# Kernel tuning notes

Measured on AMD Instinct MI355X. Metric: run time of the kernel, lower is better.

Reference implementation:

```python
import jax, jax.numpy as jnp
import numpy as np

B, L, D, H = 8, 512, 1024, 16
HD = D // H
DIST_VOCAB = 64
NEG = -1e9


def setup_inputs() -> dict:
    key = jax.random.key(0)
    ks = jax.random.split(key, 16)
    inp = {}
    inp['q'] = jax.random.normal(ks[0], (B, L, D), jnp.float32)
    inp['k'] = jax.random.normal(ks[1], (B, L, D), jnp.float32)
    inp['v'] = jax.random.normal(ks[2], (B, L, D), jnp.float32)
    s = 1.0 / np.sqrt(D)
    inp['Wq'] = jax.random.normal(ks[3], (D, D), jnp.float32) * s
    inp['bq'] = jnp.zeros((D,), jnp.float32)
    inp['Wk'] = jax.random.normal(ks[4], (D, D), jnp.float32) * s
    inp['bk'] = jnp.zeros((D,), jnp.float32)
    inp['Wv'] = jax.random.normal(ks[5], (D, D), jnp.float32) * s
    inp['bv'] = jnp.zeros((D,), jnp.float32)
    inp['Wo'] = jax.random.normal(ks[6], (D, D), jnp.float32) * s
    inp['bo'] = jnp.zeros((D,), jnp.float32)
    inp['dist_emb'] = jax.random.normal(ks[7], (DIST_VOCAB, H), jnp.float32) * (1.0 / np.sqrt(H))
    # sinusoidal positional table (1, L, D), rank-3 as asserted in AttentionBase
    pos = np.arange(L)[:, None]
    dim = np.arange(D)[None, :]
    ang = pos / np.power(10000.0, (2 * (dim // 2)) / D)
    pe = np.where(dim % 2 == 0, np.sin(ang), np.cos(ang)).astype(np.float32)
    inp['sin_enc'] = jnp.asarray(pe)[None]
    inp['length'] = jax.random.randint(ks[8], (B,), L // 2, L + 1, jnp.int32)
    inp['dist'] = jax.random.randint(ks[9], (B, L, L), 0, DIST_VOCAB, jnp.int32)
    return inp


def _rope(x, sin_pos, cos_pos):
    # x: (B, L, D). rotate-half interleaved: [-x1, x0, -x3, x2, ...]
    x_shift = jnp.stack([-x[..., 1::2], x[..., 0::2]], axis=-1).reshape(x.shape)
    return x * cos_pos + x_shift * sin_pos


def reference(q, k, v, Wq, bq, Wk, bk, Wv, bv, Wo, bo, dist_emb, sin_enc, length, dist):
    # linear projections (torch Linear: x @ W.T + b)
    qp = q @ Wq.T + bq
    kp = k @ Wk.T + bk
    vp = v @ Wv.T + bv
    # rope (pe='rope', cls_len=0, step=0)
    sin_pos = jnp.repeat(sin_enc[:, :L, 0::2], 2, axis=-1)
    cos_pos = jnp.repeat(sin_enc[:, :L, 1::2], 2, axis=-1)
    qp = _rope(qp, sin_pos, cos_pos)
    kp = _rope(kp, sin_pos, cos_pos)
    # split heads -> (B, H, L, HD)
    qh = qp.reshape(B, L, H, HD).transpose(0, 2, 1, 3)
    kh = kp.reshape(B, L, H, HD).transpose(0, 2, 1, 3)
    vh = vp.reshape(B, L, H, HD).transpose(0, 2, 1, 3)
    # scale (scale_length=0 -> 1/sqrt(d_head))
    qh = qh * (1.0 / np.sqrt(HD))
    scores = jnp.einsum('bhqd,bhkd->bhqk', qh, kh)
    # relative 'dist' bias: (B,L,L,H) -> (B,H,L,L)
    scores = scores + dist_emb[dist].transpose(0, 3, 1, 2)
    # padding mask: key positions >= valid length (future=False)
    key_mask = jnp.arange(L)[None, :] >= length[:, None]  # (B, L)
    scores = jnp.where(key_mask[:, None, None, :], NEG, scores)
    attn = jax.nn.softmax(scores, axis=-1)  # dropout p=0.0 => identity
    out = jnp.einsum('bhqk,bhkd->bhqd', attn, vh)
    out = out.transpose(0, 2, 1, 3).reshape(B, L, D)
    return out @ Wo.T + bo
```

## Files before the change

### kernel.cpp

```cpp
#include <hip/hip_runtime.h>
#include <stdint.h>

typedef unsigned short u16;
typedef __bf16 bf16x8 __attribute__((ext_vector_type(8)));
typedef float f32x4 __attribute__((ext_vector_type(4)));

#define MFMA16(a, b, c) __builtin_amdgcn_mfma_f32_16x16x32_bf16(a, b, c, 0, 0, 0)

__device__ __forceinline__ float b2f(u16 u) { return __uint_as_float(((uint32_t)u) << 16); }
__device__ __forceinline__ u16 f2b(float f) {
    uint32_t x = __float_as_uint(f);
    return (u16)((x + 0x7fffu + ((x >> 16) & 1u)) >> 16);
}
__device__ __forceinline__ void load16(const void* g, void* l) {
    __builtin_amdgcn_global_load_lds(
        (const __attribute__((address_space(1))) uint32_t*)(uintptr_t)g,
        (__attribute__((address_space(3))) uint32_t*)(uint32_t)(uintptr_t)l,
        16, 0, 0);
}
__device__ __forceinline__ bf16x8 ld8f(const float* f) {
    float4 a = *(const float4*)f;
    float4 b = *(const float4*)(f + 4);
    bf16x8 o;
    o[0] = (__bf16)a.x; o[1] = (__bf16)a.y; o[2] = (__bf16)a.z; o[3] = (__bf16)a.w;
    o[4] = (__bf16)b.x; o[5] = (__bf16)b.y; o[6] = (__bf16)b.z; o[7] = (__bf16)b.w;
    return o;
}

__global__ __launch_bounds__(256) void convert_k(
    const float* __restrict__ q, const float* __restrict__ k, const float* __restrict__ v,
    const float* __restrict__ Wq, const float* __restrict__ Wk,
    const float* __restrict__ Wv, const float* __restrict__ Wo,
    u16* __restrict__ qb, u16* __restrict__ kb, u16* __restrict__ vb,
    u16* __restrict__ wqb, u16* __restrict__ wkb, u16* __restrict__ wvb,
    u16* __restrict__ wob)
{
    const float* src; u16* dst; int n8;
    switch (blockIdx.y) {
        case 0: src = q;  dst = qb;  n8 = 524288; break;
        case 1: src = k;  dst = kb;  n8 = 524288; break;
        case 2: src = v;  dst = vb;  n8 = 524288; break;
        case 3: src = Wq; dst = wqb; n8 = 131072; break;
        case 4: src = Wk; dst = wkb; n8 = 131072; break;
        case 5: src = Wv; dst = wvb; n8 = 131072; break;
        default: src = Wo; dst = wob; n8 = 131072; break;
    }
    int i = blockIdx.x * 256 + threadIdx.x;
    if (i >= n8) return;
    bf16x8 o = ld8f(src + (size_t)i * 8);
    *(bf16x8*)(dst + (size_t)i * 8) = o;
}

__global__ __launch_bounds__(256, 6) void gemm_proj_b(
    const u16* __restrict__ qb, const u16* __restrict__ kb, const u16* __restrict__ vb,
    const u16* __restrict__ wqb, const u16* __restrict__ wkb, const u16* __restrict__ wvb,
    const float* __restrict__ bq, const float* __restrict__ bk, const float* __restrict__ bv,
    const float* __restrict__ sin_enc,
    u16* __restrict__ qh, u16* __restrict__ kh, u16* __restrict__ vt)
{
    __shared__ __align__(16) u16 lA[2][64 * 32];
    __shared__ __align__(16) u16 lB[2][128 * 32];
    const int t = threadIdx.x, wave = t >> 6, lane = t & 63;
    const int group = blockIdx.x;
    const int w_idx = group >> 6;
    const int m0 = (group & 63) << 6;
    const int n0 = blockIdx.y << 7;
    const u16* A = (w_idx == 0) ? qb : (w_idx == 1 ? kb : vb);
    const u16* W = (w_idx == 0) ? wqb : (w_idx == 1 ? wkb : wvb);
    const float* bias = (w_idx == 0) ? bq : (w_idx == 1 ? bk : bv);

    const int wr = wave >> 1, wc = wave & 1;
    const int col16 = lane & 15, g16 = lane >> 4;
    f32x4 acc[2][4] = {};

    const int cA = wave * 64 + lane;
    const u16* gA = A + (size_t)(m0 + (cA >> 2)) * 1024 + ((cA & 3) << 3);
    const int c0 = wave * 128 + lane;
    const u16* gB = W + (size_t)(n0 + (c0 >> 2)) * 1024 + ((c0 & 3) << 3);

    load16(gA, (char*)lA[0] + wave * 1024);
    load16(gB, (char*)lB[0] + wave * 2048);
    load16(gB + 16 * 1024, (char*)lB[0] + wave * 2048 + 1024);

    for (int it = 0; it < 32; ++it) {
        const int buf = it & 1, nbuf = buf ^ 1;
        __syncthreads();
        if (it + 1 < 32) {
            const int kk = (it + 1) << 5;
            load16(gA + kk, (char*)lA[nbuf] + wave * 1024);
            load16(gB + kk, (char*)lB[nbuf] + wave * 2048);
            load16(gB + kk + 16 * 1024, (char*)lB[nbuf] + wave * 2048 + 1024);
        }
        const u16* pA = lA[buf] + (wr * 32 + col16) * 32 + g16 * 8;
        const u16* pB = lB[buf] + (wc * 64 + col16) * 32 + g16 * 8;
        bf16x8 af[2], bfr[4];
#pragma unroll
        for (int i = 0; i < 2; i++) af[i] = *(const bf16x8*)(pA + i * 512);
#pragma unroll
        for (int i = 0; i < 4; i++) bfr[i] = *(const bf16x8*)(pB + i * 512);
#pragma unroll
        for (int mi = 0; mi < 2; mi++)
#pragma unroll
            for (int ni = 0; ni < 4; ni++)
                acc[mi][ni] = MFMA16(af[mi], bfr[ni], acc[mi][ni]);
    }

#pragma unroll
    for (int ni = 0; ni < 4; ni++) {
        const int n = n0 + wc * 64 + ni * 16 + col16;
        const float bn = bias[n];
        const int h = n >> 6, hd = n & 63;
#pragma unroll
        for (int mi = 0; mi < 2; mi++) {
#pragma unroll
            for (int r = 0; r < 4; r++) {
                const int m = m0 + wr * 32 + mi * 16 + g16 * 4 + r;
                const int b = m >> 9, l = m & 511;
                float x = acc[mi][ni][r] + bn;
                if (w_idx == 2) {
                    vt[((size_t)(b * 16 + h) * 64 + hd) * 512 + l] = f2b(x);
                } else {
                    float partner = __shfl_xor(x, 1);
                    float s = sin_enc[(size_t)l * 1024 + (n & ~1)];
                    float c = sin_enc[(size_t)l * 1024 + (n | 1)];
                    float y = (n & 1) ? (x * c + partner * s) : (x * c - partner * s);
                    if (w_idx == 0) y *= 0.125f;
                    u16* dst = (w_idx == 0) ? qh : kh;
                    dst[((size_t)(b * 16 + h) * 512 + l) * 64 + hd] = f2b(y);
                }
            }
        }
    }
}

__global__ __launch_bounds__(256) void gemm_proj_f32(
    const float* __restrict__ qin, const float* __restrict__ kin, const float* __restrict__ vin,
    const float* __restrict__ Wq, const float* __restrict__ bq,
    const float* __restrict__ Wk, const float* __restrict__ bk,
    const float* __restrict__ Wv, const float* __restrict__ bv,
    const float* __restrict__ sin_enc,
    u16* __restrict__ qh, u16* __restrict__ kh, u16* __restrict__ vt)
{
    __shared__ __align__(16) u16 lA[128 * 32];
    __shared__ __align__(16) u16 lB[128 * 32];
    const int t = threadIdx.x, wave = t >> 6, lane = t & 63;
    const int bx = blockIdx.x;
    const int w_idx = bx >> 3;
    const int n0 = (bx & 7) << 7;
    const int m0 = blockIdx.y << 7;
    const float* A    = (w_idx == 0) ? qin : (w_idx == 1 ? kin : vin);
    const float* W    = (w_idx == 0) ? Wq  : (w_idx == 1 ? Wk  : Wv);
    const float* bias = (w_idx == 0) ? bq  : (w_idx == 1 ? bk  : bv);

    const int wr = wave >> 1, wc = wave & 1;
    const int col16 = lane & 15, g16 = lane >> 4;
    f32x4 acc[4][4] = {};

    const int c0   = wave * 128 + lane;
    const int row0 = c0 >> 2;
    const int kp   = (c0 & 3) << 3;
    const size_t gA0 = (size_t)(m0 + row0) * 1024 + kp;
    const size_t gB0 = (size_t)(n0 + row0) * 1024 + kp;
    u16* wA0 = lA + c0 * 8;
    u16* wA1 = lA + (c0 + 64) * 8;
    u16* wB0 = lB + c0 * 8;
    u16* wB1 = lB + (c0 + 64) * 8;

    bf16x8 ra0 = ld8f(A + gA0);
    bf16x8 ra1 = ld8f(A + gA0 + 16 * 1024);
    bf16x8 rb0 = ld8f(W + gB0);
    bf16x8 rb1 = ld8f(W + gB0 + 16 * 1024);

    for (int kk = 32; kk <= 1024; kk += 32) {
        __syncthreads();
        *(bf16x8*)wA0 = ra0; *(bf16x8*)wA1 = ra1;
        *(bf16x8*)wB0 = rb0; *(bf16x8*)wB1 = rb1;
        __syncthreads();
        if (kk < 1024) {
            ra0 = ld8f(A + gA0 + kk);
            ra1 = ld8f(A + gA0 + kk + 16 * 1024);
            rb0 = ld8f(W + gB0 + kk);
            rb1 = ld8f(W + gB0 + kk + 16 * 1024);
        }
        const u16* pA = lA + (wr * 64 + col16) * 32 + g16 * 8;
        const u16* pB = lB + (wc * 64 + col16) * 32 + g16 * 8;
        bf16x8 af[4], bfr[4];
#pragma unroll
        for (int i = 0; i < 4; i++) {
            af[i]  = *(const bf16x8*)(pA + i * 512);
            bfr[i] = *(const bf16x8*)(pB + i * 512);
        }
#pragma unroll
        for (int mi = 0; mi < 4; mi++)
#pragma unroll
            for (int ni = 0; ni < 4; ni++)
                acc[mi][ni] = MFMA16(af[mi], bfr[ni], acc[mi][ni]);
    }

#pragma unroll
    for (int ni = 0; ni < 4; ni++) {
        const int n = n0 + wc * 64 + ni * 16 + col16;
        const float bn = bias[n];
        const int h = n >> 6, hd = n & 63;
#pragma unroll
        for (int mi = 0; mi < 4; mi++) {
#pragma unroll
            for (int r = 0; r < 4; r++) {
                const int m = m0 + wr * 64 + mi * 16 + g16 * 4 + r;
                const int b = m >> 9, l = m & 511;
                float x = acc[mi][ni][r] + bn;
                if (w_idx == 2) {
                    vt[((size_t)(b * 16 + h) * 64 + hd) * 512 + l] = f2b(x);
                } else {
                    float partner = __shfl_xor(x, 1);
                    float s = sin_enc[(size_t)l * 1024 + (n & ~1)];
                    float c = sin_enc[(size_t)l * 1024 + (n | 1)];
                    float y = (n & 1) ? (x * c + partner * s) : (x * c - partner * s);
                    if (w_idx == 0) y *= 0.125f;
                    u16* dst = (w_idx == 0) ? qh : kh;
                    dst[((size_t)(b * 16 + h) * 512 + l) * 64 + hd] = f2b(y);
                }
            }
        }
    }
}

__global__ __launch_bounds__(256) void attn_kernel(
    const u16* __restrict__ qh, const u16* __restrict__ kh, const u16* __restrict__ vt,
    const float* __restrict__ demb_g, const int* __restrict__ length,
    const int* __restrict__ dist, u16* __restrict__ ctx)
{
    __shared__ __align__(16) u16 Qs[64 * 64];
    __shared__ __align__(16) u16 Ks[64 * 64];
    __shared__ __align__(16) u16 Vs[64 * 64];
    __shared__ __align__(16) u16 Ps[4][16 * 64];
    __shared__ __align__(16) uint8_t Ds[64 * 64];
    __shared__ float demb[64];

    const int t = threadIdx.x, wave = t >> 6, lane = t & 63;
    const int bxx = blockIdx.x;
    const int qt = bxx & 7, bh = bxx >> 3;
    const int b = bh >> 4, h = bh & 15;
    if (t < 64) demb[t] = demb_g[t * 16 + h];
    const int len_b = length[b];
    const int ktmax = (len_b + 63) >> 6;
    const int col16 = lane & 15, g16 = lane >> 4;
    const int c0 = wave * 128 + lane, c1 = c0 + 64;

    const u16* qbase = qh + (size_t)(bh * 512 + qt * 64) * 64;
    {
        uint4 rq0 = *(const uint4*)(qbase + c0 * 8);
        uint4 rq1 = *(const uint4*)(qbase + c1 * 8);
        *(uint4*)((char*)Qs + c0 * 16) = rq0;
        *(uint4*)((char*)Qs + c1 * 16) = rq1;
    }

    const u16* kbase = kh + (size_t)bh * 512 * 64;
    const u16* vbase = vt + (size_t)bh * 64 * 512;
    const int qrow_base = qt * 64 + wave * 16 + g16 * 4;

    const int drow = t >> 2;
    const int dcol = (t & 3) << 4;
    const int* dg = dist + (size_t)b * 512 * 512 + (size_t)(qt * 64 + drow) * 512 + dcol;
    uint32_t* DsW = (uint32_t*)(Ds + drow * 64 + dcol);

    uint4 rk0 = *(const uint4*)(kbase + c0 * 8);
    uint4 rk1 = *(const uint4*)(kbase + c1 * 8);
    uint4 rv0 = *(const uint4*)(vbase + (size_t)(c0 >> 3) * 512 + (c0 & 7) * 8);
    uint4 rv1 = *(const uint4*)(vbase + (size_t)(c1 >> 3) * 512 + (c1 & 7) * 8);
    int4 dd[4];
#pragma unroll
    for (int j = 0; j < 4; j++) dd[j] = *(const int4*)(dg + j * 4);

    __syncthreads();
    const u16* pQ = Qs + (wave * 16 + col16) * 64 + g16 * 8;
    const bf16x8 qa0 = *(const bf16x8*)pQ;
    const bf16x8 qa1 = *(const bf16x8*)(pQ + 32);

    f32x4 oacc[4] = {};
    float mrow[4], lrow[4];
#pragma unroll
    for (int r = 0; r < 4; r++) { mrow[r] = -1e30f; lrow[r] = 0.f; }

    for (int kt = 0; kt < ktmax; kt++) {
        __syncthreads();
        *(uint4*)((char*)Ks + c0 * 16) = rk0;
        *(uint4*)((char*)Ks + c1 * 16) = rk1;
        *(uint4*)((char*)Vs + c0 * 16) = rv0;
        *(uint4*)((char*)Vs + c1 * 16) = rv1;
#pragma unroll
        for (int j = 0; j < 4; j++)
            DsW[j] = (uint32_t)(dd[j].x & 63) | ((uint32_t)(dd[j].y & 63) << 8) |
                     ((uint32_t)(dd[j].z & 63) << 16) | ((uint32_t)(dd[j].w & 63) << 24);
        __syncthreads();
        if (kt + 1 < ktmax) {
            const u16* kb = kbase + (size_t)(kt + 1) * 64 * 64;
            rk0 = *(const uint4*)(kb + c0 * 8);
            rk1 = *(const uint4*)(kb + c1 * 8);
            rv0 = *(const uint4*)(vbase + (size_t)(c0 >> 3) * 512 + (kt + 1) * 64 + (c0 & 7) * 8);
            rv1 = *(const uint4*)(vbase + (size_t)(c1 >> 3) * 512 + (kt + 1) * 64 + (c1 & 7) * 8);
            const int* dgn = dg + (kt + 1) * 64;
#pragma unroll
            for (int j = 0; j < 4; j++) dd[j] = *(const int4*)(dgn + j * 4);
        }

        f32x4 sacc[4] = {};
#pragma unroll
        for (int ni = 0; ni < 4; ni++) {
            const u16* pK = Ks + (ni * 16 + col16) * 64 + g16 * 8;
            bf16x8 kf0 = *(const bf16x8*)pK;
            bf16x8 kf1 = *(const bf16x8*)(pK + 32);
            sacc[ni] = MFMA16(qa0, kf0, sacc[ni]);
            sacc[ni] = MFMA16(qa1, kf1, sacc[ni]);
        }

        float rmax[4] = {-1e30f, -1e30f, -1e30f, -1e30f};
        const int qrl = wave * 16 + g16 * 4;
#pragma unroll
        for (int ni = 0; ni < 4; ni++) {
            const int kcl = ni * 16 + col16;
            const bool masked = (kt * 64 + kcl) >= len_b;
#pragma unroll
            for (int r = 0; r < 4; r++) {
                float s = sacc[ni][r] + demb[Ds[(qrl + r) * 64 + kcl]];
                s = masked ? -1e9f : s;
                sacc[ni][r] = s;
                rmax[r] = fmaxf(rmax[r], s);
            }
        }
#pragma unroll
        for (int off = 1; off < 16; off <<= 1)
#pragma unroll
            for (int r = 0; r < 4; r++) rmax[r] = fmaxf(rmax[r], __shfl_xor(rmax[r], off));

        float alpha[4], rsum[4];
#pragma unroll
        for (int r = 0; r < 4; r++) {
            float mn = fmaxf(mrow[r], rmax[r]);
            alpha[r] = __expf(mrow[r] - mn);
            mrow[r] = mn;
            rsum[r] = 0.f;
        }
#pragma unroll
        for (int ni = 0; ni < 4; ni++)
#pragma unroll
            for (int r = 0; r < 4; r++) {
                float p = __expf(sacc[ni][r] - mrow[r]);
                sacc[ni][r] = p;
                rsum[r] += p;
            }
#pragma unroll
        for (int off = 1; off < 16; off <<= 1)
#pragma unroll
            for (int r = 0; r < 4; r++) rsum[r] += __shfl_xor(rsum[r], off);
#pragma unroll
        for (int r = 0; r < 4; r++) lrow[r] = lrow[r] * alpha[r] + rsum[r];
#pragma unroll
        for (int di = 0; di < 4; di++)
#pragma unroll
            for (int r = 0; r < 4; r++) oacc[di][r] *= alpha[r];

        u16* Pw = &Ps[wave][0];
#pragma unroll
        for (int ni = 0; ni < 4; ni++)
#pragma unroll
            for (int r = 0; r < 4; r++)
                Pw[(g16 * 4 + r) * 64 + ni * 16 + col16] = f2b(sacc[ni][r]);

        const u16* pP = Pw + col16 * 64 + g16 * 8;
        bf16x8 pa0 = *(const bf16x8*)pP;
        bf16x8 pa1 = *(const bf16x8*)(pP + 32);
#pragma unroll
        for (int di = 0; di < 4; di++) {
            const u16* pV = Vs + (di * 16 + col16) * 64 + g16 * 8;
            bf16x8 vf0 = *(const bf16x8*)pV;
            bf16x8 vf1 = *(const bf16x8*)(pV + 32);
            oacc[di] = MFMA16(pa0, vf0, oacc[di]);
            oacc[di] = MFMA16(pa1, vf1, oacc[di]);
        }
    }

#pragma unroll
    for (int di = 0; di < 4; di++)
#pragma unroll
        for (int r = 0; r < 4; r++) {
            const int qrow = qrow_base + r;
            const int d = di * 16 + col16;
            const float inv_l = 1.0f / fmaxf(lrow[r], 1e-30f);
            ctx[(size_t)(b * 512 + qrow) * 1024 + h * 64 + d] = f2b(oacc[di][r] * inv_l);
        }
}

__global__ __launch_bounds__(256, 4) void gemm_out_b(
    const u16* __restrict__ ctx, const u16* __restrict__ wob,
    const float* __restrict__ bo, float* __restrict__ out)
{
    __shared__ __align__(16) u16 lA[2][64 * 32];
    __shared__ __align__(16) u16 lB[2][64 * 32];
    const int t = threadIdx.x, wave = t >> 6, lane = t & 63;
    const int m0 = blockIdx.x << 6;
    const int n0 = blockIdx.y << 6;
    const int wr = wave >> 1, wc = wave & 1;
    const int col16 = lane & 15, g16 = lane >> 4;
    f32x4 acc[2][2] = {};

    const int cA = wave * 64 + lane;
    const u16* gA = ctx + (size_t)(m0 + (cA >> 2)) * 1024 + ((cA & 3) << 3);
    const u16* gB = wob + (size_t)(n0 + (cA >> 2)) * 1024 + ((cA & 3) << 3);

    load16(gA, (char*)lA[0] + wave * 1024);
    load16(gB, (char*)lB[0] + wave * 1024);

    for (int it = 0; it < 32; ++it) {
        const int buf = it & 1, nbuf = buf ^ 1;
        __syncthreads();
        if (it + 1 < 32) {
            const int kk = (it + 1) << 5;
            load16(gA + kk, (char*)lA[nbuf] + wave * 1024);
            load16(gB + kk, (char*)lB[nbuf] + wave * 1024);
        }
        const u16* pA = lA[buf] + (wr * 32 + col16) * 32 + g16 * 8;
        const u16* pB = lB[buf] + (wc * 32 + col16) * 32 + g16 * 8;
        bf16x8 af[2], bfr[2];
#pragma unroll
        for (int i = 0; i < 2; i++) {
            af[i]  = *(const bf16x8*)(pA + i * 512);
            bfr[i] = *(const bf16x8*)(pB + i * 512);
        }
#pragma unroll
        for (int mi = 0; mi < 2; mi++)
#pragma unroll
            for (int ni = 0; ni < 2; ni++)
                acc[mi][ni] = MFMA16(af[mi], bfr[ni], acc[mi][ni]);
    }

#pragma unroll
    for (int ni = 0; ni < 2; ni++) {
        const int n = n0 + wc * 32 + ni * 16 + col16;
        const float bn = bo[n];
#pragma unroll
        for (int mi = 0; mi < 2; mi++)
#pragma unroll
            for (int r = 0; r < 4; r++) {
                const int m = m0 + wr * 32 + mi * 16 + g16 * 4 + r;
                out[(size_t)m * 1024 + n] = acc[mi][ni][r] + bn;
            }
    }
}

__global__ __launch_bounds__(256) void gemm_out_f32(
    const u16* __restrict__ ctx, const float* __restrict__ Wo,
    const float* __restrict__ bo, float* __restrict__ out)
{
    __shared__ __align__(16) u16 lA[128 * 32];
    __shared__ __align__(16) u16 lB[128 * 32];
    const int t = threadIdx.x, wave = t >> 6, lane = t & 63;
    const int n0 = blockIdx.x << 7;
    const int m0 = blockIdx.y << 7;
    const int wr = wave >> 1, wc = wave & 1;
    const int col16 = lane & 15, g16 = lane >> 4;
    f32x4 acc[4][4] = {};

    const int c0   = wave * 128 + lane;
    const int row0 = c0 >> 2;
    const int kp   = (c0 & 3) << 3;
    const u16* gA = ctx + (size_t)(m0 + row0) * 1024 + kp;
    const size_t gB0 = (size_t)(n0 + row0) * 1024 + kp;
    u16* wA0 = lA + c0 * 8;
    u16* wA1 = lA + (c0 + 64) * 8;
    u16* wB0 = lB + c0 * 8;
    u16* wB1 = lB + (c0 + 64) * 8;

    uint4 ua0 = *(const uint4*)gA;
    uint4 ua1 = *(const uint4*)(gA + 16 * 1024);
    bf16x8 ra0 = *(bf16x8*)&ua0, ra1 = *(bf16x8*)&ua1;
    bf16x8 rb0 = ld8f(Wo + gB0);
    bf16x8 rb1 = ld8f(Wo + gB0 + 16 * 1024);

    for (int kk = 32; kk <= 1024; kk += 32) {
        __syncthreads();
        *(bf16x8*)wA0 = ra0; *(bf16x8*)wA1 = ra1;
        *(bf16x8*)wB0 = rb0; *(bf16x8*)wB1 = rb1;
        __syncthreads();
        if (kk < 1024) {
            uint4 t0 = *(const uint4*)(gA + kk);
            uint4 t1 = *(const uint4*)(gA + kk + 16 * 1024);
            ra0 = *(bf16x8*)&t0; ra1 = *(bf16x8*)&t1;
            rb0 = ld8f(Wo + gB0 + kk);
            rb1 = ld8f(Wo + gB0 + kk + 16 * 1024);
        }
        const u16* pA = lA + (wr * 64 + col16) * 32 + g16 * 8;
        const u16* pB = lB + (wc * 64 + col16) * 32 + g16 * 8;
        bf16x8 af[4], bfr[4];
#pragma unroll
        for (int i = 0; i < 4; i++) {
            af[i]  = *(const bf16x8*)(pA + i * 512);
            bfr[i] = *(const bf16x8*)(pB + i * 512);
        }
#pragma unroll
        for (int mi = 0; mi < 4; mi++)
#pragma unroll
            for (int ni = 0; ni < 4; ni++)
                acc[mi][ni] = MFMA16(af[mi], bfr[ni], acc[mi][ni]);
    }

#pragma unroll
    for (int ni = 0; ni < 4; ni++) {
        const int n = n0 + wc * 64 + ni * 16 + col16;
        const float bn = bo[n];
#pragma unroll
        for (int mi = 0; mi < 4; mi++)
#pragma unroll
            for (int r = 0; r < 4; r++) {
                const int m = m0 + wr * 64 + mi * 16 + g16 * 4 + r;
                out[(size_t)m * 1024 + n] = acc[mi][ni][r] + bn;
            }
    }
}

extern "C" void kernel_launch(void* const* d_in, const int* in_sizes, int n_in,
                              void* d_out, int out_size, void* d_ws, size_t ws_size,
                              hipStream_t stream) {
    const float* q       = (const float*)d_in[0];
    const float* k       = (const float*)d_in[1];
    const float* v       = (const float*)d_in[2];
    const float* Wq      = (const float*)d_in[3];
    const float* bq      = (const float*)d_in[4];
    const float* Wk      = (const float*)d_in[5];
    const float* bk      = (const float*)d_in[6];
    const float* Wv      = (const float*)d_in[7];
    const float* bv      = (const float*)d_in[8];
    const float* Wo      = (const float*)d_in[9];
    const float* bo      = (const float*)d_in[10];
    const float* demb    = (const float*)d_in[11];
    const float* sin_enc = (const float*)d_in[12];
    const int* length    = (const int*)d_in[13];
    const int* dist      = (const int*)d_in[14];

    const size_t SLOT = 4194304;
    u16* qh  = (u16*)d_ws;
    u16* kh  = qh + SLOT;
    u16* vt  = kh + SLOT;
    u16* ctx = vt + SLOT;

    if (ws_size >= (size_t)64 * 1024 * 1024) {
        u16* qb  = ctx + SLOT;
        u16* kb  = qb + SLOT;
        u16* vb  = kb + SLOT;
        u16* wqb = vb + SLOT;
        u16* wkb = wqb + 1048576;
        u16* wvb = wkb + 1048576;
        u16* wob = wvb + 1048576;
        convert_k<<<dim3(2048, 7), 256, 0, stream>>>(q, k, v, Wq, Wk, Wv, Wo,
                                                     qb, kb, vb, wqb, wkb, wvb, wob);
        gemm_proj_b<<<dim3(192, 8), 256, 0, stream>>>(qb, kb, vb, wqb, wkb, wvb,
                                                      bq, bk, bv, sin_enc, qh, kh, vt);
        attn_kernel<<<dim3(1024), 256, 0, stream>>>(qh, kh, vt, demb, length, dist, ctx);
        gemm_out_b<<<dim3(64, 16), 256, 0, stream>>>(ctx, wob, bo, (float*)d_out);
    } else {
        gemm_proj_f32<<<dim3(24, 32), 256, 0, stream>>>(q, k, v, Wq, bq, Wk, bk, Wv, bv,
                                                        sin_enc, qh, kh, vt);
        attn_kernel<<<dim3(1024), 256, 0, stream>>>(qh, kh, vt, demb, length, dist, ctx);
        gemm_out_f32<<<dim3(8, 32), 256, 0, stream>>>(ctx, Wo, bo, (float*)d_out);
    }
}
```

Before: 254.5 us.

## Replace LDS-staged projection GEMMs with register-direct global loads and larger tiles

Both bf16 GEMMs (the QKV projection and the output projection) no longer stage tiles through LDS with double buffering and barriers. Each lane now loads its MFMA fragments straight from global memory into registers, with software prefetch of the next k-slice. Tiles grow to 128x128 for the projection and 64x128 for the output, and occupancy bounds are lowered to match. This removes LDS traffic and __syncthreads, but operands are no longer shared across waves in the block, so each wave fetches more from global memory and cache, and the larger tiles use more registers.

Result: slower. 338.4 us (+33.0%).

```diff
diff --git a/kernel.cpp b/kernel.cpp
--- a/kernel.cpp
+++ b/kernel.cpp
@@ -12,11 +12,9 @@
     uint32_t x = __float_as_uint(f);
     return (u16)((x + 0x7fffu + ((x >> 16) & 1u)) >> 16);
 }
-__device__ __forceinline__ void load16(const void* g, void* l) {
-    __builtin_amdgcn_global_load_lds(
-        (const __attribute__((address_space(1))) uint32_t*)(uintptr_t)g,
-        (__attribute__((address_space(3))) uint32_t*)(uint32_t)(uintptr_t)l,
-        16, 0, 0);
+__device__ __forceinline__ bf16x8 ldg8(const u16* p) {
+    uint4 r = *(const uint4*)p;
+    return *(bf16x8*)&r;
 }
 __device__ __forceinline__ bf16x8 ld8f(const float* f) {
     float4 a = *(const float4*)f;
@@ -51,19 +49,17 @@
     *(bf16x8*)(dst + (size_t)i * 8) = o;
 }
 
-__global__ __launch_bounds__(256, 6) void gemm_proj_b(
+__global__ __launch_bounds__(256, 3) void gemm_proj_r(
     const u16* __restrict__ qb, const u16* __restrict__ kb, const u16* __restrict__ vb,
     const u16* __restrict__ wqb, const u16* __restrict__ wkb, const u16* __restrict__ wvb,
     const float* __restrict__ bq, const float* __restrict__ bk, const float* __restrict__ bv,
     const float* __restrict__ sin_enc,
     u16* __restrict__ qh, u16* __restrict__ kh, u16* __restrict__ vt)
 {
-    __shared__ __align__(16) u16 lA[2][64 * 32];
-    __shared__ __align__(16) u16 lB[2][128 * 32];
     const int t = threadIdx.x, wave = t >> 6, lane = t & 63;
     const int group = blockIdx.x;
-    const int w_idx = group >> 6;
-    const int m0 = (group & 63) << 6;
+    const int w_idx = group >> 5;
+    const int m0 = (group & 31) << 7;
     const int n0 = blockIdx.y << 7;
     const u16* A = (w_idx == 0) ? qb : (w_idx == 1 ? kb : vb);
     const u16* W = (w_idx == 0) ? wqb : (w_idx == 1 ? wkb : wvb);
@@ -71,52 +67,54 @@
 
     const int wr = wave >> 1, wc = wave & 1;
     const int col16 = lane & 15, g16 = lane >> 4;
-    f32x4 acc[2][4] = {};
-
-    const int cA = wave * 64 + lane;
-    const u16* gA = A + (size_t)(m0 + (cA >> 2)) * 1024 + ((cA & 3) << 3);
-    const int c0 = wave * 128 + lane;
-    const u16* gB = W + (size_t)(n0 + (c0 >> 2)) * 1024 + ((c0 & 3) << 3);
-
-    load16(gA, (char*)lA[0] + wave * 1024);
-    load16(gB, (char*)lB[0] + wave * 2048);
-    load16(gB + 16 * 1024, (char*)lB[0] + wave * 2048 + 1024);
-
-    for (int it = 0; it < 32; ++it) {
-        const int buf = it & 1, nbuf = buf ^ 1;
-        __syncthreads();
-        if (it + 1 < 32) {
-            const int kk = (it + 1) << 5;
-            load16(gA + kk, (char*)lA[nbuf] + wave * 1024);
-            load16(gB + kk, (char*)lB[nbuf] + wave * 2048);
-            load16(gB + kk + 16 * 1024, (char*)lB[nbuf] + wave * 2048 + 1024);
-        }
-        const u16* pA = lA[buf] + (wr * 32 + col16) * 32 + g16 * 8;
-        const u16* pB = lB[buf] + (wc * 64 + col16) * 32 + g16 * 8;
-        bf16x8 af[2], bfr[4];
-#pragma unroll
-        for (int i = 0; i < 2; i++) af[i] = *(const bf16x8*)(pA + i * 512);
-#pragma unroll
-        for (int i = 0; i < 4; i++) bfr[i] = *(const bf16x8*)(pB + i * 512);
-#pragma unroll
-        for (int mi = 0; mi < 2; mi++)
+    f32x4 acc[4][4] = {};
+
+    const u16* pa = A + (size_t)(m0 + wr * 64 + col16) * 1024 + g16 * 8;
+    const u16* pb = W + (size_t)(n0 + wc * 64 + col16) * 1024 + g16 * 8;
+
+    bf16x8 ac[4], bc[4], an[4], bn[4];
+#pragma unroll
+    for (int i = 0; i < 4; i++) {
+        ac[i] = ldg8(pa + i * 16384);
+        bc[i] = ldg8(pb + i * 16384);
+    }
+    for (int kk = 0; kk < 1024; kk += 64) {
+#pragma unroll
+        for (int i = 0; i < 4; i++) {
+            an[i] = ldg8(pa + i * 16384 + kk + 32);
+            bn[i] = ldg8(pb + i * 16384 + kk + 32);
+        }
+#pragma unroll
+        for (int mi = 0; mi < 4; mi++)
 #pragma unroll
             for (int ni = 0; ni < 4; ni++)
-                acc[mi][ni] = MFMA16(af[mi], bfr[ni], acc[mi][ni]);
+                acc[mi][ni] = MFMA16(ac[mi], bc[ni], acc[mi][ni]);
+        if (kk + 64 < 1024) {
+#pragma unroll
+            for (int i = 0; i < 4; i++) {
+                ac[i] = ldg8(pa + i * 16384 + kk + 64);
+                bc[i] = ldg8(pb + i * 16384 + kk + 64);
+            }
+        }
+#pragma unroll
+        for (int mi = 0; mi < 4; mi++)
+#pragma unroll
+            for (int ni = 0; ni < 4; ni++)
+                acc[mi][ni] = MFMA16(an[mi], bn[ni], acc[mi][ni]);
     }
 
 #pragma unroll
     for (int ni = 0; ni < 4; ni++) {
         const int n = n0 + wc * 64 + ni * 16 + col16;
-        const float bn = bias[n];
+        const float bn_ = bias[n];
         const int h = n >> 6, hd = n & 63;
 #pragma unroll
-        for (int mi = 0; mi < 2; mi++) {
+        for (int mi = 0; mi < 4; mi++) {
 #pragma unroll
             for (int r = 0; r < 4; r++) {
-                const int m = m0 + wr * 32 + mi * 16 + g16 * 4 + r;
+                const int m = m0 + wr * 64 + mi * 16 + g16 * 4 + r;
                 const int b = m >> 9, l = m & 511;
-                float x = acc[mi][ni][r] + bn;
+                float x = acc[mi][ni][r] + bn_;
                 if (w_idx == 2) {
                     vt[((size_t)(b * 16 + h) * 64 + hd) * 512 + l] = f2b(x);
                 } else {
@@ -391,59 +389,58 @@
         }
 }
 
-__global__ __launch_bounds__(256, 4) void gemm_out_b(
+__global__ __launch_bounds__(256, 4) void gemm_out_r(
     const u16* __restrict__ ctx, const u16* __restrict__ wob,
     const float* __restrict__ bo, float* __restrict__ out)
 {
-    __shared__ __align__(16) u16 lA[2][64 * 32];
-    __shared__ __align__(16) u16 lB[2][64 * 32];
     const int t = threadIdx.x, wave = t >> 6, lane = t & 63;
     const int m0 = blockIdx.x << 6;
-    const int n0 = blockIdx.y << 6;
+    const int n0 = blockIdx.y << 7;
     const int wr = wave >> 1, wc = wave & 1;
     const int col16 = lane & 15, g16 = lane >> 4;
-    f32x4 acc[2][2] = {};
-
-    const int cA = wave * 64 + lane;
-    const u16* gA = ctx + (size_t)(m0 + (cA >> 2)) * 1024 + ((cA & 3) << 3);
-    const u16* gB = wob + (size_t)(n0 + (cA >> 2)) * 1024 + ((cA & 3) << 3);
-
-    load16(gA, (char*)lA[0] + wave * 1024);
-    load16(gB, (char*)lB[0] + wave * 1024);
-
-    for (int it = 0; it < 32; ++it) {
-        const int buf = it & 1, nbuf = buf ^ 1;
-        __syncthreads();
-        if (it + 1 < 32) {
-            const int kk = (it + 1) << 5;
-            load16(gA + kk, (char*)lA[nbuf] + wave * 1024);
-            load16(gB + kk, (char*)lB[nbuf] + wave * 1024);
-        }
-        const u16* pA = lA[buf] + (wr * 32 + col16) * 32 + g16 * 8;
-        const u16* pB = lB[buf] + (wc * 32 + col16) * 32 + g16 * 8;
-        bf16x8 af[2], bfr[2];
-#pragma unroll
-        for (int i = 0; i < 2; i++) {
-            af[i]  = *(const bf16x8*)(pA + i * 512);
-            bfr[i] = *(const bf16x8*)(pB + i * 512);
-        }
+    f32x4 acc[2][4] = {};
+
+    const u16* pa = ctx + (size_t)(m0 + wr * 32 + col16) * 1024 + g16 * 8;
+    const u16* pb = wob + (size_t)(n0 + wc * 64 + col16) * 1024 + g16 * 8;
+
+    bf16x8 ac[2], bc[4], an[2], bn[4];
+#pragma unroll
+    for (int i = 0; i < 2; i++) ac[i] = ldg8(pa + i * 16384);
+#pragma unroll
+    for (int i = 0; i < 4; i++) bc[i] = ldg8(pb + i * 16384);
+    for (int kk = 0; kk < 1024; kk += 64) {
+#pragma unroll
+        for (int i = 0; i < 2; i++) an[i] = ldg8(pa + i * 16384 + kk + 32);
+#pragma unroll
+        for (int i = 0; i < 4; i++) bn[i] = ldg8(pb + i * 16384 + kk + 32);
 #pragma unroll
         for (int mi = 0; mi < 2; mi++)
 #pragma unroll
-            for (int ni = 0; ni < 2; ni++)
-                acc[mi][ni] = MFMA16(af[mi], bfr[ni], acc[mi][ni]);
-    }
-
-#pragma unroll
-    for (int ni = 0; ni < 2; ni++) {
-        const int n = n0 + wc * 32 + ni * 16 + col16;
-        const float bn = bo[n];
+            for (int ni = 0; ni < 4; ni++)
+                acc[mi][ni] = MFMA16(ac[mi], bc[ni], acc[mi][ni]);
+        if (kk + 64 < 1024) {
+#pragma unroll
+            for (int i = 0; i < 2; i++) ac[i] = ldg8(pa + i * 16384 + kk + 64);
+#pragma unroll
+            for (int i = 0; i < 4; i++) bc[i] = ldg8(pb + i * 16384 + kk + 64);
+        }
+#pragma unroll
+        for (int mi = 0; mi < 2; mi++)
+#pragma unroll
+            for (int ni = 0; ni < 4; ni++)
+                acc[mi][ni] = MFMA16(an[mi], bn[ni], acc[mi][ni]);
+    }
+
+#pragma unroll
+    for (int ni = 0; ni < 4; ni++) {
+        const int n = n0 + wc * 64 + ni * 16 + col16;
+        const float bn_ = bo[n];
 #pragma unroll
         for (int mi = 0; mi < 2; mi++)
 #pragma unroll
             for (int r = 0; r < 4; r++) {
                 const int m = m0 + wr * 32 + mi * 16 + g16 * 4 + r;
-                out[(size_t)m * 1024 + n] = acc[mi][ni][r] + bn;
+                out[(size_t)m * 1024 + n] = acc[mi][ni][r] + bn_;
             }
     }
 }
@@ -553,10 +550,10 @@
         u16* wob = wvb + 1048576;
         convert_k<<<dim3(2048, 7), 256, 0, stream>>>(q, k, v, Wq, Wk, Wv, Wo,
                                                      qb, kb, vb, wqb, wkb, wvb, wob);
-        gemm_proj_b<<<dim3(192, 8), 256, 0, stream>>>(qb, kb, vb, wqb, wkb, wvb,
-                                                      bq, bk, bv, sin_enc, qh, kh, vt);
+        gemm_proj_r<<<dim3(96, 8), 256, 0, stream>>>(qb, kb, vb, wqb, wkb, wvb,
+                                                     bq, bk, bv, sin_enc, qh, kh, vt);
         attn_kernel<<<dim3(1024), 256, 0, stream>>>(qh, kh, vt, demb, length, dist, ctx);
-        gemm_out_b<<<dim3(64, 16), 256, 0, stream>>>(ctx, wob, bo, (float*)d_out);
+        gemm_out_r<<<dim3(64, 8), 256, 0, stream>>>(ctx, wob, bo, (float*)d_out);
     } else {
         gemm_proj_f32<<<dim3(24, 32), 256, 0, stream>>>(q, k, v, Wq, bq, Wk, bk, Wv, bv,
                                                         sin_enc, qh, kh, vt);
```
